# Kernel optimization log

Measured on AMD Instinct MI355X. Metric: run time of the kernel, lower is better.

The kernel has to match this reference:

```python
import jax, jax.numpy as jnp
import numpy as np
from jax import lax

DN = ('NCHW', 'OIHW', 'NCHW')
NUM_IN_CAPS = 1152  # 32 * 6 * 6
NUM_OUT_CAPS = 10
IN_CAP_DIM = 8
OUT_CAP_DIM = 16
ROUTING_ITERS = 3


def squash(x):
    # unit_v * |x|^2 / (1 + |x|^2), norm over last dim
    n = jnp.linalg.norm(x, axis=-1, keepdims=True)
    return (x / n) * (n * n / (1.0 + n * n))


def setup_inputs() -> dict:
    key = jax.random.key(0)
    ks = jax.random.split(key, 12)
    B = 256
    return {
        'x': jax.random.normal(ks[0], (B, 1, 28, 28), jnp.float32),
        'conv1_w': jax.random.normal(ks[1], (256, 1, 9, 9), jnp.float32) * 0.05,
        'conv1_b': jnp.zeros((256,), jnp.float32),
        'pconv_w': jax.random.normal(ks[2], (256, 256, 9, 9), jnp.float32) * 0.02,
        'pconv_b': jnp.zeros((256,), jnp.float32),
        'W_caps': jax.random.normal(ks[3], (NUM_IN_CAPS, NUM_OUT_CAPS, OUT_CAP_DIM, IN_CAP_DIM), jnp.float32),
        'dec_w1': jax.random.normal(ks[4], (160, 512), jnp.float32) * 0.05,
        'dec_b1': jnp.zeros((512,), jnp.float32),
        'dec_w2': jax.random.normal(ks[5], (512, 1024), jnp.float32) * 0.04,
        'dec_b2': jnp.zeros((1024,), jnp.float32),
        'dec_w3': jax.random.normal(ks[6], (1024, 784), jnp.float32) * 0.03,
        'dec_b3': jnp.zeros((784,), jnp.float32),
    }


def reference(x, conv1_w, conv1_b, pconv_w, pconv_b, W_caps,
              dec_w1, dec_b1, dec_w2, dec_b2, dec_w3, dec_b3):
    # conv1: 1 -> 256, k9, s1, no activation (faithful to source)
    h = lax.conv_general_dilated(x, conv1_w, (1, 1), 'VALID', dimension_numbers=DN)
    h = h + conv1_b[None, :, None, None]  # (B,256,20,20)
    # primary caps conv: 256 -> 32*8, k9, s2
    h = lax.conv_general_dilated(h, pconv_w, (2, 2), 'VALID', dimension_numbers=DN)
    h = h + pconv_b[None, :, None, None]  # (B,256,6,6)
    B = h.shape[0]
    u_in = squash(h.reshape(B, -1, IN_CAP_DIM))  # (B,1152,8)
    # prediction vectors u_hat: (B,1152,10,16)
    u = jnp.einsum('ijab,nib->nija', W_caps, u_in)
    # routing-by-agreement; b is shared across batch and accumulates batch-summed agreement (faithful)
    b = jnp.zeros((NUM_IN_CAPS, NUM_OUT_CAPS), u.dtype)
    v = None
    for r in range(ROUTING_ITERS + 1):
        c = jax.nn.softmax(b, axis=-1)             # (1152,10)
        s = jnp.einsum('ij,nija->nja', c, u)        # (B,10,16)
        v = squash(s)
        if r < ROUTING_ITERS:
            b = b + jnp.einsum('nija,nja->ij', u, v)
    # decoder path: mask by predicted class
    logits = jnp.linalg.norm(v, axis=-1)            # (B,10)
    label = jnp.argmax(logits, axis=1)
    one_hot = jax.nn.one_hot(label, NUM_OUT_CAPS, dtype=v.dtype)
    recon = (one_hot[..., None] * v).reshape(B, NUM_OUT_CAPS * OUT_CAP_DIM)
    recon = jax.nn.relu(recon @ dec_w1 + dec_b1)
    recon = jax.nn.relu(recon @ dec_w2 + dec_b2)
    recon = jax.nn.sigmoid(recon @ dec_w3 + dec_b3)  # (B,784)
    return (v, recon)
```

## Files before the change

kernel.cpp:

```cpp
#include <hip/hip_runtime.h>
#include <hip/hip_fp16.h>
#include <math.h>


typedef __attribute__((ext_vector_type(8))) _Float16 half8;
typedef __attribute__((ext_vector_type(8))) short short8;
typedef __attribute__((ext_vector_type(4))) float floatx4;

__device__ __forceinline__ unsigned short f16bits(float v) {
    _Float16 h = (_Float16)v;
    unsigned short b;
    __builtin_memcpy(&b, &h, 2);
    return b;
}
__device__ __forceinline__ float f16back(unsigned short b) {
    _Float16 h;
    __builtin_memcpy(&h, &b, 2);
    return (float)h;
}
__device__ __forceinline__ void load_lds16(const void* g, void* l) {
    __builtin_amdgcn_global_load_lds(
        (const __attribute__((address_space(1))) unsigned int*)g,
        (__attribute__((address_space(3))) unsigned int*)l, 16, 0, 0);
}

__global__ __launch_bounds__(256, 2) void conv1_kernel(
    const float* __restrict__ x, const float* __restrict__ w,
    const float* __restrict__ bias, unsigned short* __restrict__ xpack)
{
    __shared__ float xs[784];
    __shared__ float wl[64 * 81];
    int t = threadIdx.x;
    int n = blockIdx.x;
    int cot = blockIdx.y;

    for (int j = t; j < 784; j += 256) xs[j] = x[n * 784 + j];
    {
        int co_s = t >> 2, k0 = (t & 3) * 21;
        const float* wsrc = w + (size_t)(cot * 64 + co_s) * 81;
        #pragma unroll
        for (int k = 0; k < 21; ++k)
            if (k0 + k < 81) wl[co_s * 81 + k0 + k] = wsrc[k0 + k];
    }
    __syncthreads();

    int co_l = t & 63, slot = t >> 6;
    int co = cot * 64 + co_l;
    float bv = bias[co];
    for (int r5 = 0; r5 < 5; ++r5) {
        int py = slot * 5 + r5;
        float acc[20];
        #pragma unroll
        for (int i = 0; i < 20; i++) acc[i] = bv;
        #pragma unroll
        for (int ky = 0; ky < 9; ++ky) {
            float xr[28];
            const float4* rowp = (const float4*)&xs[(py + ky) * 28];
            #pragma unroll
            for (int q = 0; q < 7; q++) {
                float4 v4 = rowp[q];
                xr[4*q] = v4.x; xr[4*q+1] = v4.y; xr[4*q+2] = v4.z; xr[4*q+3] = v4.w;
            }
            #pragma unroll
            for (int kx = 0; kx < 9; ++kx) {
                float wv = wl[co_l * 81 + ky * 9 + kx];
                #pragma unroll
                for (int px = 0; px < 20; ++px) acc[px] += wv * xr[px + kx];
            }
        }
        #pragma unroll
        for (int px = 0; px < 20; ++px) {
            float v = acc[px];
            unsigned short h = f16bits(v);
            unsigned short l = f16bits(v - f16back(h));
            size_t pix = (size_t)n * 400 + py * 20 + px;
            xpack[pix * 512 + co] = h;
            xpack[pix * 512 + 256 + co] = l;
        }
    }
}

__global__ __launch_bounds__(256) void wpack_kernel(
    const float* __restrict__ w, unsigned short* __restrict__ wp)
{
    int tid = blockIdx.x * 256 + threadIdx.x;
    if (tid >= 648 * 16 * 64) return;
    int lane = tid & 63, g = (tid >> 6) & 15, gs = tid >> 10;
    int cb = gs & 7, kk = gs >> 3;
    int ky = kk / 9, kx = kk - ky * 9;
    int n16 = lane & 15, q = lane >> 4;
    int co = g * 16 + n16;
    unsigned short hv[8];
    #pragma unroll
    for (int j = 0; j < 8; ++j) {
        int ci = cb * 32 + q * 8 + j;
        hv[j] = f16bits(w[((size_t)co * 256 + ci) * 81 + ky * 9 + kx]);
    }
    unsigned short* dst = wp + ((size_t)gs * 16 + g) * 512 + lane * 8;
    *(short8*)dst = *(short8*)hv;
}

__global__ __launch_bounds__(256, 2) void pconv_mfma_kernel(
    const unsigned short* __restrict__ xp, const unsigned short* __restrict__ wp,
    __half* __restrict__ P3)
{
    __shared__ unsigned char lds[32768];
    int t = threadIdx.x;
    int lane = t & 63;
    int w = __builtin_amdgcn_readfirstlane(t >> 6);
    int mtile = blockIdx.x, kc = blockIdx.y;
    int m16 = lane & 15, q = lane >> 4;

    unsigned int asrc[2];
    #pragma unroll
    for (int j = 0; j < 2; ++j) {
        int r = w * 16 + j * 8 + (lane >> 3);
        int m = mtile * 64 + r;
        int n = m / 36, pos = m - n * 36;
        int oy = pos / 6, ox = pos - oy * 6;
        int pixbase = n * 400 + oy * 40 + ox * 2;
        int pp = (lane & 7) ^ (lane >> 3);
        int partoff = (pp < 4) ? pp * 16 : 512 + (pp - 4) * 16;
        asrc[j] = (unsigned int)(pixbase * 1024 + partoff);
    }
    const char* xb = (const char*)xp;
    const char* wb = (const char*)wp;

    floatx4 acc[4][4];
    #pragma unroll
    for (int a = 0; a < 4; ++a)
        #pragma unroll
        for (int b = 0; b < 4; ++b) acc[a][b] = (floatx4){0.f, 0.f, 0.f, 0.f};

    int slot_hi = (q ^ (m16 & 7)) * 16;
    int slot_lo = slot_hi ^ 64;

    auto stageP = [&](int p, int buf) {
        #pragma unroll
        for (int e = 0; e < 2; ++e) {
            int s = 2 * p + e; if (s > 215) s = 215;
            int gs = kc * 216 + s;
            int kk = gs >> 3, cb = gs & 7;
            int ky = kk / 9, kx = kk - ky * 9;
            unsigned int delta = (unsigned int)((ky * 20 + kx) * 1024 + cb * 64);
            #pragma unroll
            for (int j = 0; j < 2; ++j)
                load_lds16(xb + asrc[j] + delta,
                           (void*)(lds + buf * 16384 + e * 8192 + w * 2048 + j * 1024));
        }
    };
    auto loadB = [&](int s, half8* B) {
        if (s > 215) s = 215;
        int gs = kc * 216 + s;
        #pragma unroll
        for (int c = 0; c < 4; ++c)
            B[c] = *(const half8*)(wb + ((size_t)gs * 16 + (w * 4 + c)) * 1024 + lane * 16);
    };
    auto compute = [&](int buf, int e, half8* B) {
        #pragma unroll
        for (int ms = 0; ms < 4; ++ms) {
            const char* base = (const char*)lds + buf * 16384 + e * 8192 + (ms * 16 + m16) * 128;
            half8 Ah = *(const half8*)(base + slot_hi);
            half8 Al = *(const half8*)(base + slot_lo);
            #pragma unroll
            for (int c = 0; c < 4; ++c) {
                acc[ms][c] = __builtin_amdgcn_mfma_f32_16x16x32_f16(Ah, B[c], acc[ms][c], 0, 0, 0);
                acc[ms][c] = __builtin_amdgcn_mfma_f32_16x16x32_f16(Al, B[c], acc[ms][c], 0, 0, 0);
            }
        }
    };

    half8 Bcur[4], Bnext[4];
    stageP(0, 0);
    loadB(0, Bcur);
    __syncthreads();
    for (int p = 0; p < 108; ++p) {
        int buf = p & 1;
        stageP(p + 1, buf ^ 1);
        loadB(2 * p + 1, Bnext);
        compute(buf, 0, Bcur);
        loadB(2 * p + 2, Bcur);
        compute(buf, 1, Bnext);
        __syncthreads();
    }

    __half* outp = P3 + ((size_t)kc * 9216 + (size_t)mtile * 64) * 256;
    #pragma unroll
    for (int ms = 0; ms < 4; ++ms)
        #pragma unroll
        for (int r = 0; r < 4; ++r) {
            int ml = ms * 16 + q * 4 + r;
            #pragma unroll
            for (int c = 0; c < 4; ++c) {
                int co = w * 64 + c * 16 + m16;
                outp[ml * 256 + co] = __float2half(acc[ms][c][r]);
            }
        }
}

__global__ __launch_bounds__(256) void squash_u_kernel(
    const __half* __restrict__ P3, const float* __restrict__ pb, float* __restrict__ u)
{
    int cap = blockIdx.x * 256 + threadIdx.x;
    int n = cap / 1152;
    int capl = cap - n * 1152;
    float z[8]; float n2 = 0.f;
    #pragma unroll
    for (int b = 0; b < 8; ++b) {
        int q2 = capl * 8 + b;
        int co = q2 / 36;
        int pos = q2 - co * 36;
        int m = n * 36 + pos;
        float s = 0.f;
        #pragma unroll
        for (int kc = 0; kc < 3; ++kc)
            s += __half2float(P3[((size_t)kc * 9216 + m) * 256 + co]);
        s += pb[co];
        z[b] = s; n2 += s * s;
    }
    float sc = sqrtf(n2) / (1.0f + n2);
    float4* op = (float4*)(u + (size_t)cap * 8);
    op[0] = make_float4(z[0]*sc, z[1]*sc, z[2]*sc, z[3]*sc);
    op[1] = make_float4(z[4]*sc, z[5]*sc, z[6]*sc, z[7]*sc);
}

__global__ __launch_bounds__(256, 2) void s_kernel(
    const float* __restrict__ b, const float* __restrict__ u,
    const float* __restrict__ W, float* __restrict__ sbuf)
{
    __shared__ float cs[24][10];
    int t = threadIdx.x;
    int a = t & 15, nl = t >> 4;
    int nt = blockIdx.x;
    int bz = blockIdx.y;
    int i0 = bz * 24;
    int n0 = nt * 32 + nl * 2;

    if (t < 24) {
        int i = i0 + t;
        float e[10], m = -1e30f;
        #pragma unroll
        for (int j = 0; j < 10; j++) { e[j] = b[i * 10 + j]; m = fmaxf(m, e[j]); }
        float sum = 0.f;
        #pragma unroll
        for (int j = 0; j < 10; j++) { e[j] = expf(e[j] - m); sum += e[j]; }
        float inv = 1.f / sum;
        #pragma unroll
        for (int j = 0; j < 10; j++) cs[t][j] = e[j] * inv;
    }
    __syncthreads();

    float acc[2][10];
    #pragma unroll
    for (int r = 0; r < 2; ++r)
        #pragma unroll
        for (int j = 0; j < 10; ++j) acc[r][j] = 0.f;

    for (int i = i0; i < i0 + 24; ++i) {
        float4 u0[2], u1[2];
        #pragma unroll
        for (int r = 0; r < 2; ++r) {
            const float4* up = (const float4*)&u[(size_t)(n0 + r) * 9216 + (size_t)i * 8];
            u0[r] = up[0]; u1[r] = up[1];
        }
        #pragma unroll
        for (int j = 0; j < 10; ++j) {
            const float4* wpt = (const float4*)&W[(((size_t)i * 10 + j) * 16 + a) * 8];
            float4 w0 = wpt[0], w1 = wpt[1];
            float cij = cs[i - i0][j];
            #pragma unroll
            for (int r = 0; r < 2; ++r) {
                float d = w0.x*u0[r].x + w0.y*u0[r].y + w0.z*u0[r].z + w0.w*u0[r].w
                        + w1.x*u1[r].x + w1.y*u1[r].y + w1.z*u1[r].z + w1.w*u1[r].w;
                acc[r][j] += cij * d;
            }
        }
    }
    #pragma unroll
    for (int r = 0; r < 2; ++r)
        #pragma unroll
        for (int j = 0; j < 10; ++j)
            sbuf[(size_t)bz * 40960 + (((size_t)(n0 + r) * 10 + j) * 16) + a] = acc[r][j];
}

__global__ __launch_bounds__(256) void squash_v_kernel(const float* __restrict__ sbuf,
                                float* __restrict__ v, float* __restrict__ vout)
{
    int t = threadIdx.x;
    int a = t & 15;
    int idx = blockIdx.x * 16 + (t >> 4);
    float s = 0.f;
    #pragma unroll
    for (int z = 0; z < 48; ++z) s += sbuf[(size_t)z * 40960 + idx * 16 + a];
    float n2 = s * s;
    n2 += __shfl_xor(n2, 1);
    n2 += __shfl_xor(n2, 2);
    n2 += __shfl_xor(n2, 4);
    n2 += __shfl_xor(n2, 8);
    float sc = sqrtf(n2) / (1.0f + n2);
    float y = s * sc;
    v[idx * 16 + a] = y;
    if (vout) vout[idx * 16 + a] = y;
}

__global__ __launch_bounds__(192) void bupd_kernel(
    const float* __restrict__ u, const float* __restrict__ v,
    const float* __restrict__ W, float* __restrict__ b)
{
    int i0 = blockIdx.x * 4;
    int n0 = blockIdx.y * 128;
    int t = threadIdx.x;
    if (t >= 160) return;
    int j = t >> 4, a = t & 15;
    float g4[4][8];
    #pragma unroll
    for (int g = 0; g < 4; ++g)
        #pragma unroll
        for (int k = 0; k < 8; ++k) g4[g][k] = 0.f;

    for (int n = n0; n < n0 + 128; ++n) {
        float vv = v[n * 160 + t];
        const float4* ub = (const float4*)&u[(size_t)n * 9216 + (size_t)i0 * 8];
        #pragma unroll
        for (int g = 0; g < 4; ++g) {
            float4 q0 = ub[g * 2], q1 = ub[g * 2 + 1];
            g4[g][0] += q0.x * vv; g4[g][1] += q0.y * vv; g4[g][2] += q0.z * vv; g4[g][3] += q0.w * vv;
            g4[g][4] += q1.x * vv; g4[g][5] += q1.y * vv; g4[g][6] += q1.z * vv; g4[g][7] += q1.w * vv;
        }
    }
    #pragma unroll
    for (int g = 0; g < 4; ++g) {
        int i = i0 + g;
        const float4* wpt = (const float4*)&W[(((size_t)i * 10 + j) * 16 + a) * 8];
        float4 w0 = wpt[0], w1 = wpt[1];
        float p = w0.x*g4[g][0] + w0.y*g4[g][1] + w0.z*g4[g][2] + w0.w*g4[g][3]
                + w1.x*g4[g][4] + w1.y*g4[g][5] + w1.z*g4[g][6] + w1.w*g4[g][7];
        p += __shfl_xor(p, 1);
        p += __shfl_xor(p, 2);
        p += __shfl_xor(p, 4);
        p += __shfl_xor(p, 8);
        if (a == 0) atomicAdd(&b[i * 10 + j], p);
    }
}

__global__ void mask_kernel(const float* __restrict__ v, float* __restrict__ out)
{
    int n = threadIdx.x;
    const float* vp = &v[n * 160];
    int best = 0; float bestv = -1.f;
    for (int j = 0; j < 10; j++) {
        float n2 = 0.f;
        #pragma unroll
        for (int a = 0; a < 16; a++) { float y = vp[j * 16 + a]; n2 += y * y; }
        float ln = sqrtf(n2);
        if (ln > bestv) { bestv = ln; best = j; }
    }
    for (int j = 0; j < 10; j++)
        for (int a = 0; a < 16; a++)
            out[n * 160 + j * 16 + a] = (j == best) ? vp[j * 16 + a] : 0.f;
}

template<int K, int KCH, int O>
__global__ __launch_bounds__(256, 2) void mlp_part_kernel(
    const float* __restrict__ X, const float* __restrict__ Wm,
    float* __restrict__ partial)
{
    __shared__ float XS[KCH * 16];
    int t = threadIdx.x;
    int og = t & 63, ns = t >> 6;
    int n0 = blockIdx.x * 16;
    int o = blockIdx.y * 256 + og * 4;
    int o_c = min(o, O - 4);
    int ks = blockIdx.z;
    int kc0 = ks * KCH;

    for (int idx = t; idx < KCH * 16; idx += 256) {
        int k_l = idx >> 4, n_l = idx & 15;
        XS[k_l * 16 + n_l] = X[(size_t)(n0 + n_l) * K + kc0 + k_l];
    }
    __syncthreads();

    float acc[4][4];
    #pragma unroll
    for (int r = 0; r < 4; ++r)
        #pragma unroll
        for (int q = 0; q < 4; ++q) acc[r][q] = 0.f;

    #pragma unroll 8
    for (int k = 0; k < KCH; ++k) {
        float4 wv = *(const float4*)&Wm[(size_t)(kc0 + k) * O + o_c];
        float4 xs4 = *(const float4*)&XS[k * 16 + ns * 4];
        acc[0][0] += xs4.x * wv.x; acc[0][1] += xs4.x * wv.y; acc[0][2] += xs4.x * wv.z; acc[0][3] += xs4.x * wv.w;
        acc[1][0] += xs4.y * wv.x; acc[1][1] += xs4.y * wv.y; acc[1][2] += xs4.y * wv.z; acc[1][3] += xs4.y * wv.w;
        acc[2][0] += xs4.z * wv.x; acc[2][1] += xs4.z * wv.y; acc[2][2] += xs4.z * wv.z; acc[2][3] += xs4.z * wv.w;
        acc[3][0] += xs4.w * wv.x; acc[3][1] += xs4.w * wv.y; acc[3][2] += xs4.w * wv.z; acc[3][3] += xs4.w * wv.w;
    }

    if (o < O) {
        float* pp = partial + ((size_t)ks * 256 + n0 + ns * 4) * O + o;
        #pragma unroll
        for (int r = 0; r < 4; ++r)
            *(float4*)(pp + (size_t)r * O) = make_float4(acc[r][0], acc[r][1], acc[r][2], acc[r][3]);
    }
}

template<int KS, int O, int ACT>
__global__ __launch_bounds__(256) void mlp_reduce_kernel(
    const float* __restrict__ partial, const float* __restrict__ bias,
    float* __restrict__ out)
{
    int n = blockIdx.y;
    int o = (blockIdx.x * 256 + threadIdx.x) * 4;
    if (o >= O) return;
    float4 s = make_float4(0.f, 0.f, 0.f, 0.f);
    #pragma unroll
    for (int ks = 0; ks < KS; ++ks) {
        float4 p = *(const float4*)&partial[((size_t)ks * 256 + n) * O + o];
        s.x += p.x; s.y += p.y; s.z += p.z; s.w += p.w;
    }
    float4 bv = *(const float4*)&bias[o];
    float r[4] = {s.x + bv.x, s.y + bv.y, s.z + bv.z, s.w + bv.w};
    #pragma unroll
    for (int q = 0; q < 4; ++q)
        r[q] = (ACT == 0) ? fmaxf(r[q], 0.f) : (1.f / (1.f + expf(-r[q])));
    *(float4*)&out[(size_t)n * O + o] = make_float4(r[0], r[1], r[2], r[3]);
}

extern "C" void kernel_launch(void* const* d_in, const int* in_sizes, int n_in,
                              void* d_out, int out_size, void* d_ws, size_t ws_size,
                              hipStream_t stream)
{
    const float* x       = (const float*)d_in[0];
    const float* conv1_w = (const float*)d_in[1];
    const float* conv1_b = (const float*)d_in[2];
    const float* pconv_w = (const float*)d_in[3];
    const float* pconv_b = (const float*)d_in[4];
    const float* W_caps  = (const float*)d_in[5];
    const float* dec_w1  = (const float*)d_in[6];
    const float* dec_b1  = (const float*)d_in[7];
    const float* dec_w2  = (const float*)d_in[8];
    const float* dec_b2  = (const float*)d_in[9];
    const float* dec_w3  = (const float*)d_in[10];
    const float* dec_b3  = (const float*)d_in[11];
    float* out = (float*)d_out;

    float* ws = (float*)d_ws;
    size_t off = 0;
    auto alloc = [&](size_t nf) { float* p = ws + off; off += (nf + 63) & ~(size_t)63; return p; };
    unsigned short* xpack = (unsigned short*)alloc(26214400);
    unsigned short* wpack = (unsigned short*)alloc(2654208);
    __half* P3  = (__half*)alloc(3538944);
    float* u_in = alloc(2359296);
    float* bbuf = alloc(11520);
    float* sbuf = alloc(48 * 40960);
    float* vbuf = alloc(40960);
    float* rin  = alloc(40960);
    float* mpart = alloc(8 * 256 * 1024);
    float* h1   = alloc(131072);
    float* h2   = alloc(262144);

    hipMemsetAsync(bbuf, 0, 11520 * sizeof(float), stream);

    wpack_kernel<<<(648 * 16 * 64 + 255) / 256, 256, 0, stream>>>(pconv_w, wpack);
    conv1_kernel<<<dim3(256, 4), 256, 0, stream>>>(x, conv1_w, conv1_b, xpack);
    pconv_mfma_kernel<<<dim3(144, 3), 256, 0, stream>>>(xpack, wpack, P3);
    squash_u_kernel<<<1152, 256, 0, stream>>>(P3, pconv_b, u_in);

    for (int r = 0; r < 4; ++r) {
        s_kernel<<<dim3(8, 48), 256, 0, stream>>>(bbuf, u_in, W_caps, sbuf);
        squash_v_kernel<<<160, 256, 0, stream>>>(sbuf, vbuf, (r == 3) ? out : nullptr);
        if (r < 3) bupd_kernel<<<dim3(288, 2), 192, 0, stream>>>(u_in, vbuf, W_caps, bbuf);
    }

    mask_kernel<<<1, 256, 0, stream>>>(vbuf, rin);

    mlp_part_kernel<160, 80, 512><<<dim3(16, 2, 2), 256, 0, stream>>>(rin, dec_w1, mpart);
    mlp_reduce_kernel<2, 512, 0><<<dim3(1, 256), 256, 0, stream>>>(mpart, dec_b1, h1);
    mlp_part_kernel<512, 128, 1024><<<dim3(16, 4, 4), 256, 0, stream>>>(h1, dec_w2, mpart);
    mlp_reduce_kernel<4, 1024, 0><<<dim3(1, 256), 256, 0, stream>>>(mpart, dec_b2, h2);
    mlp_part_kernel<1024, 128, 784><<<dim3(16, 4, 8), 256, 0, stream>>>(h2, dec_w3, mpart);
    mlp_reduce_kernel<8, 784, 1><<<dim3(1, 256), 256, 0, stream>>>(mpart, dec_b3, out + 40960);
}
```

Baseline: 763.6 us.

## Split pconv K six ways, parallelize mask, fuse MLP reduce into next layer

The primary-caps MFMA conv now splits K into 6 chunks instead of 3, giving 864 blocks and allowing 3 blocks per CU, at the cost of twice as many fp16 partials for squash_u to sum. The mask kernel moves from one thread per sample to 16 lanes per sample with a shuffle reduction across 16 blocks. The decoder MLP drops the separate reduce kernels: each layer's load stage sums the previous layer's partials, adds bias and applies ReLU, with larger K chunks. This cuts three launches and the intermediate round trips.

```diff
diff --git a/kernel.cpp b/kernel.cpp
--- a/kernel.cpp
+++ b/kernel.cpp
@@ -100,9 +100,9 @@
     *(short8*)dst = *(short8*)hv;
 }
 
-__global__ __launch_bounds__(256, 2) void pconv_mfma_kernel(
+__global__ __launch_bounds__(256, 3) void pconv_mfma_kernel(
     const unsigned short* __restrict__ xp, const unsigned short* __restrict__ wp,
-    __half* __restrict__ P3)
+    __half* __restrict__ P6)
 {
     __shared__ unsigned char lds[32768];
     int t = threadIdx.x;
@@ -138,8 +138,8 @@
     auto stageP = [&](int p, int buf) {
         #pragma unroll
         for (int e = 0; e < 2; ++e) {
-            int s = 2 * p + e; if (s > 215) s = 215;
-            int gs = kc * 216 + s;
+            int s = 2 * p + e; if (s > 107) s = 107;
+            int gs = kc * 108 + s;
             int kk = gs >> 3, cb = gs & 7;
             int ky = kk / 9, kx = kk - ky * 9;
             unsigned int delta = (unsigned int)((ky * 20 + kx) * 1024 + cb * 64);
@@ -150,8 +150,8 @@
         }
     };
     auto loadB = [&](int s, half8* B) {
-        if (s > 215) s = 215;
-        int gs = kc * 216 + s;
+        if (s > 107) s = 107;
+        int gs = kc * 108 + s;
         #pragma unroll
         for (int c = 0; c < 4; ++c)
             B[c] = *(const half8*)(wb + ((size_t)gs * 16 + (w * 4 + c)) * 1024 + lane * 16);
@@ -174,7 +174,7 @@
     stageP(0, 0);
     loadB(0, Bcur);
     __syncthreads();
-    for (int p = 0; p < 108; ++p) {
+    for (int p = 0; p < 54; ++p) {
         int buf = p & 1;
         stageP(p + 1, buf ^ 1);
         loadB(2 * p + 1, Bnext);
@@ -184,7 +184,7 @@
         __syncthreads();
     }
 
-    __half* outp = P3 + ((size_t)kc * 9216 + (size_t)mtile * 64) * 256;
+    __half* outp = P6 + ((size_t)kc * 9216 + (size_t)mtile * 64) * 256;
     #pragma unroll
     for (int ms = 0; ms < 4; ++ms)
         #pragma unroll
@@ -199,7 +199,7 @@
 }
 
 __global__ __launch_bounds__(256) void squash_u_kernel(
-    const __half* __restrict__ P3, const float* __restrict__ pb, float* __restrict__ u)
+    const __half* __restrict__ P6, const float* __restrict__ pb, float* __restrict__ u)
 {
     int cap = blockIdx.x * 256 + threadIdx.x;
     int n = cap / 1152;
@@ -213,8 +213,8 @@
         int m = n * 36 + pos;
         float s = 0.f;
         #pragma unroll
-        for (int kc = 0; kc < 3; ++kc)
-            s += __half2float(P3[((size_t)kc * 9216 + m) * 256 + co]);
+        for (int kc = 0; kc < 6; ++kc)
+            s += __half2float(P6[((size_t)kc * 9216 + m) * 256 + co]);
         s += pb[co];
         z[b] = s; n2 += s * s;
     }
@@ -343,21 +343,26 @@
     }
 }
 
-__global__ void mask_kernel(const float* __restrict__ v, float* __restrict__ out)
-{
-    int n = threadIdx.x;
+__global__ __launch_bounds__(256) void mask_kernel(const float* __restrict__ v, float* __restrict__ out)
+{
+    int t = threadIdx.x;
+    int a = t & 15, nl = t >> 4;
+    int n = blockIdx.x * 16 + nl;
     const float* vp = &v[n * 160];
-    int best = 0; float bestv = -1.f;
-    for (int j = 0; j < 10; j++) {
-        float n2 = 0.f;
-        #pragma unroll
-        for (int a = 0; a < 16; a++) { float y = vp[j * 16 + a]; n2 += y * y; }
-        float ln = sqrtf(n2);
-        if (ln > bestv) { bestv = ln; best = j; }
-    }
-    for (int j = 0; j < 10; j++)
-        for (int a = 0; a < 16; a++)
-            out[n * 160 + j * 16 + a] = (j == best) ? vp[j * 16 + a] : 0.f;
+    int best = 0; float bestn2 = -1.f;
+    #pragma unroll
+    for (int j = 0; j < 10; ++j) {
+        float y = vp[j * 16 + a];
+        float n2 = y * y;
+        n2 += __shfl_xor(n2, 1);
+        n2 += __shfl_xor(n2, 2);
+        n2 += __shfl_xor(n2, 4);
+        n2 += __shfl_xor(n2, 8);
+        if (n2 > bestn2) { bestn2 = n2; best = j; }
+    }
+    #pragma unroll
+    for (int j = 0; j < 10; ++j)
+        out[n * 160 + j * 16 + a] = (j == best) ? vp[j * 16 + a] : 0.f;
 }
 
 template<int K, int KCH, int O>
@@ -377,6 +382,54 @@
     for (int idx = t; idx < KCH * 16; idx += 256) {
         int k_l = idx >> 4, n_l = idx & 15;
         XS[k_l * 16 + n_l] = X[(size_t)(n0 + n_l) * K + kc0 + k_l];
+    }
+    __syncthreads();
+
+    float acc[4][4];
+    #pragma unroll
+    for (int r = 0; r < 4; ++r)
+        #pragma unroll
+        for (int q = 0; q < 4; ++q) acc[r][q] = 0.f;
+
+    #pragma unroll 8
+    for (int k = 0; k < KCH; ++k) {
+        float4 wv = *(const float4*)&Wm[(size_t)(kc0 + k) * O + o_c];
+        float4 xs4 = *(const float4*)&XS[k * 16 + ns * 4];
+        acc[0][0] += xs4.x * wv.x; acc[0][1] += xs4.x * wv.y; acc[0][2] += xs4.x * wv.z; acc[0][3] += xs4.x * wv.w;
+        acc[1][0] += xs4.y * wv.x; acc[1][1] += xs4.y * wv.y; acc[1][2] += xs4.y * wv.z; acc[1][3] += xs4.y * wv.w;
+        acc[2][0] += xs4.z * wv.x; acc[2][1] += xs4.z * wv.y; acc[2][2] += xs4.z * wv.z; acc[2][3] += xs4.z * wv.w;
+        acc[3][0] += xs4.w * wv.x; acc[3][1] += xs4.w * wv.y; acc[3][2] += xs4.w * wv.z; acc[3][3] += xs4.w * wv.w;
+    }
+
+    if (o < O) {
+        float* pp = partial + ((size_t)ks * 256 + n0 + ns * 4) * O + o;
+        #pragma unroll
+        for (int r = 0; r < 4; ++r)
+            *(float4*)(pp + (size_t)r * O) = make_float4(acc[r][0], acc[r][1], acc[r][2], acc[r][3]);
+    }
+}
+
+template<int K, int KCH, int O, int PRE_KS>
+__global__ __launch_bounds__(256, 2) void mlp_part_pre_kernel(
+    const float* __restrict__ Xpart, const float* __restrict__ bprev,
+    const float* __restrict__ Wm, float* __restrict__ partial)
+{
+    __shared__ float XS[KCH * 16];
+    int t = threadIdx.x;
+    int og = t & 63, ns = t >> 6;
+    int n0 = blockIdx.x * 16;
+    int o = blockIdx.y * 256 + og * 4;
+    int o_c = min(o, O - 4);
+    int ks = blockIdx.z;
+    int kc0 = ks * KCH;
+
+    for (int idx = t; idx < KCH * 16; idx += 256) {
+        int k_l = idx >> 4, n_l = idx & 15;
+        float s = bprev[kc0 + k_l];
+        #pragma unroll
+        for (int pk = 0; pk < PRE_KS; ++pk)
+            s += Xpart[((size_t)pk * 256 + n0 + n_l) * K + kc0 + k_l];
+        XS[k_l * 16 + n_l] = fmaxf(s, 0.f);
     }
     __syncthreads();
 
@@ -449,22 +502,22 @@
     auto alloc = [&](size_t nf) { float* p = ws + off; off += (nf + 63) & ~(size_t)63; return p; };
     unsigned short* xpack = (unsigned short*)alloc(26214400);
     unsigned short* wpack = (unsigned short*)alloc(2654208);
-    __half* P3  = (__half*)alloc(3538944);
+    __half* P6  = (__half*)alloc(7077888);
     float* u_in = alloc(2359296);
     float* bbuf = alloc(11520);
     float* sbuf = alloc(48 * 40960);
     float* vbuf = alloc(40960);
     float* rin  = alloc(40960);
-    float* mpart = alloc(8 * 256 * 1024);
-    float* h1   = alloc(131072);
-    float* h2   = alloc(262144);
+    float* mp1  = alloc(1 * 256 * 512);
+    float* mp2  = alloc(2 * 256 * 1024);
+    float* mp3  = alloc(4 * 256 * 784);
 
     hipMemsetAsync(bbuf, 0, 11520 * sizeof(float), stream);
 
     wpack_kernel<<<(648 * 16 * 64 + 255) / 256, 256, 0, stream>>>(pconv_w, wpack);
     conv1_kernel<<<dim3(256, 4), 256, 0, stream>>>(x, conv1_w, conv1_b, xpack);
-    pconv_mfma_kernel<<<dim3(144, 3), 256, 0, stream>>>(xpack, wpack, P3);
-    squash_u_kernel<<<1152, 256, 0, stream>>>(P3, pconv_b, u_in);
+    pconv_mfma_kernel<<<dim3(144, 6), 256, 0, stream>>>(xpack, wpack, P6);
+    squash_u_kernel<<<1152, 256, 0, stream>>>(P6, pconv_b, u_in);
 
     for (int r = 0; r < 4; ++r) {
         s_kernel<<<dim3(8, 48), 256, 0, stream>>>(bbuf, u_in, W_caps, sbuf);
@@ -472,12 +525,10 @@
         if (r < 3) bupd_kernel<<<dim3(288, 2), 192, 0, stream>>>(u_in, vbuf, W_caps, bbuf);
     }
 
-    mask_kernel<<<1, 256, 0, stream>>>(vbuf, rin);
-
-    mlp_part_kernel<160, 80, 512><<<dim3(16, 2, 2), 256, 0, stream>>>(rin, dec_w1, mpart);
-    mlp_reduce_kernel<2, 512, 0><<<dim3(1, 256), 256, 0, stream>>>(mpart, dec_b1, h1);
-    mlp_part_kernel<512, 128, 1024><<<dim3(16, 4, 4), 256, 0, stream>>>(h1, dec_w2, mpart);
-    mlp_reduce_kernel<4, 1024, 0><<<dim3(1, 256), 256, 0, stream>>>(mpart, dec_b2, h2);
-    mlp_part_kernel<1024, 128, 784><<<dim3(16, 4, 8), 256, 0, stream>>>(h2, dec_w3, mpart);
-    mlp_reduce_kernel<8, 784, 1><<<dim3(1, 256), 256, 0, stream>>>(mpart, dec_b3, out + 40960);
-}
+    mask_kernel<<<16, 256, 0, stream>>>(vbuf, rin);
+
+    mlp_part_kernel<160, 160, 512><<<dim3(16, 2, 1), 256, 0, stream>>>(rin, dec_w1, mp1);
+    mlp_part_pre_kernel<512, 256, 1024, 1><<<dim3(16, 4, 2), 256, 0, stream>>>(mp1, dec_b1, dec_w2, mp2);
+    mlp_part_pre_kernel<1024, 256, 784, 2><<<dim3(16, 4, 4), 256, 0, stream>>>(mp2, dec_b2, dec_w3, mp3);
+    mlp_reduce_kernel<4, 784, 1><<<dim3(1, 256), 256, 0, stream>>>(mp3, dec_b3, out + 40960);
+}
```

Measured after the change: 797.4 us. 1.04x slower.
